# Kernel tuning notes

Hardware: AMD Instinct MI355X
Metric: run time of the kernel (lower is better)

## Reference

```python
import jax, jax.numpy as jnp
import numpy as np


def setup_inputs() -> dict:
    key = jax.random.key(0)
    ks = jax.random.split(key, 6)
    B, S, D, E, F, C = 4, 2048, 1024, 8, 4096, 512
    return {
        "x": jax.random.normal(ks[0], (B, S, D), dtype=jnp.float32),
        "router": jax.random.normal(ks[1], (D, E), dtype=jnp.float32) * (1.0 / np.sqrt(D)),
        "w1": jax.random.normal(ks[2], (E, D, F), dtype=jnp.float32) * (1.0 / np.sqrt(D)),
        "b1": jnp.zeros((E, F), dtype=jnp.float32),
        "w2": jax.random.normal(ks[3], (E, F, D), dtype=jnp.float32) * (1.0 / np.sqrt(F)),
        "b2": jnp.zeros((E, D), dtype=jnp.float32),
        "capacity": C,
    }


def reference(x, router, w1, b1, w2, b2, capacity):
    # x: (B,S,D); router: (D,E); per-expert FFN weights stacked on E.
    B, S, D = x.shape
    # Gate: softmax over experts, then each expert picks its top-C tokens.
    logits = jnp.einsum('bsd,de->bse', x, router)            # (B,S,E)
    affinity = jax.nn.softmax(logits, axis=-1)               # (B,S,E)
    gating, index = jax.lax.top_k(jnp.transpose(affinity, (0, 2, 1)), capacity)  # (B,E,C)
    # Dispatch: gather token features per (expert, slot). Equivalent to the
    # one-hot einsum 'becs,bsd->becd' in the original (same math, true gather).
    x_in = jax.vmap(lambda xb, ib: xb[ib])(x, index)         # (B,E,C,D)
    # Per-expert GPT2 FFN: Linear -> GELU -> Linear (grouped GEMMs over E).
    h = jax.nn.gelu(jnp.einsum('becd,edf->becf', x_in, w1) + b1[None, :, None, :],
                    approximate=False)                        # (B,E,C,F)
    x_e = jnp.einsum('becf,efd->becd', h, w2) + b2[None, :, None, :]  # (B,E,C,D)
    # Combine: weighted scatter-add back to token positions. Equivalent to
    # einsum 'becs,bec,becd->bsd' with the one-hot dispatch mask.
    weighted = gating[..., None] * x_e                       # (B,E,C,D)
    out = jax.vmap(
        lambda ib, vb: jnp.zeros((S, D), x.dtype).at[ib.reshape(-1)].add(vb.reshape(-1, D))
    )(index, weighted)                                       # (B,S,D)
    return out
```

## Files before the change

kernel.cpp:

```cpp
#include <hip/hip_runtime.h>
#include <hip/hip_bf16.h>

#define B_ 4
#define S_ 2048
#define D_ 1024
#define E_ 8
#define F_ 4096
#define C_ 512
#define BE_ (B_*E_)

typedef __attribute__((ext_vector_type(8))) short bf16x8;
typedef __attribute__((ext_vector_type(4))) float f32x4;
typedef unsigned short u16;

#define MFMA16 __builtin_amdgcn_mfma_f32_16x16x32_bf16

static constexpr size_t OFF_AFF  = 0;
static constexpr size_t OFF_IDX  = 262144;
static constexpr size_t OFF_GATE = 327680;
static constexpr size_t OFF_XIN  = 393216;
static constexpr size_t OFF_WT1  = OFF_XIN + (size_t)BE_*C_*D_*2;
static constexpr size_t OFF_WT2  = OFF_WT1 + (size_t)E_*F_*D_*2;
static constexpr size_t OFF_H    = OFF_WT2 + (size_t)E_*D_*F_*2;
static constexpr size_t WS_NEED  = OFF_H   + (size_t)BE_*C_*F_*2;

static __device__ __forceinline__ u16 f2bf(float x) {
  __hip_bfloat16 h = __float2bfloat16(x);
  return *reinterpret_cast<u16*>(&h);
}

static __device__ __forceinline__ float gelu_fast(float v) {
  float y = 1.5957691216f * (v + 0.044715f * v * v * v);
  return v / (1.0f + __expf(-y));
}

static __device__ __forceinline__ void gload16(const void* g, void* l) {
  __builtin_amdgcn_global_load_lds(
      (const __attribute__((address_space(1))) unsigned int*)g,
      (__attribute__((address_space(3))) unsigned int*)l, 16, 0, 0);
}

__global__ void router_kernel(const float* __restrict__ x,
                              const float* __restrict__ router,
                              float* __restrict__ aff) {
  int t = blockIdx.x;
  int b = t / S_, s = t % S_;
  int lane = threadIdx.x;
  const float* xrow = x + (size_t)t * D_;
  float acc[E_];
#pragma unroll
  for (int e = 0; e < E_; ++e) acc[e] = 0.f;
  for (int i = 0; i < D_/64; ++i) {
    int d = lane + i*64;
    float xv = xrow[d];
    const float* r = router + (size_t)d * E_;
#pragma unroll
    for (int e = 0; e < E_; ++e) acc[e] += xv * r[e];
  }
#pragma unroll
  for (int e = 0; e < E_; ++e) {
    float v = acc[e];
    for (int off = 32; off; off >>= 1) v += __shfl_down(v, off);
    acc[e] = v;
  }
  if (lane == 0) {
    float mx = acc[0];
#pragma unroll
    for (int e = 1; e < E_; ++e) mx = fmaxf(mx, acc[e]);
    float ev[E_]; float sum = 0.f;
#pragma unroll
    for (int e = 0; e < E_; ++e) { ev[e] = expf(acc[e] - mx); sum += ev[e]; }
    float inv = 1.0f / sum;
#pragma unroll
    for (int e = 0; e < E_; ++e) aff[((size_t)(b*E_ + e))*S_ + s] = ev[e]*inv;
  }
}

__global__ void topk_kernel(const float* __restrict__ aff,
                            int* __restrict__ idxb, float* __restrict__ gateb) {
  __shared__ unsigned long long keys[S_];
  int be = blockIdx.x;
  const float* a = aff + (size_t)be * S_;
  int tid = threadIdx.x;
  for (int i = tid; i < S_; i += 1024) {
    unsigned vb = __float_as_uint(a[i]);
    keys[i] = ((unsigned long long)(~vb) << 32) | (unsigned)i;
  }
  __syncthreads();
  for (int k = 2; k <= S_; k <<= 1) {
    for (int j = k >> 1; j > 0; j >>= 1) {
      for (int i = tid; i < S_; i += 1024) {
        int ixj = i ^ j;
        if (ixj > i) {
          unsigned long long ka = keys[i], kb = keys[ixj];
          bool up = ((i & k) == 0);
          if ((ka > kb) == up) { keys[i] = kb; keys[ixj] = ka; }
        }
      }
      __syncthreads();
    }
  }
  for (int c = tid; c < C_; c += 1024) {
    unsigned long long kk = keys[c];
    idxb[be*C_ + c]  = (int)(kk & 0xffffffffu);
    gateb[be*C_ + c] = __uint_as_float(~(unsigned)(kk >> 32));
  }
}

__global__ void gather_kernel(const float* __restrict__ x,
                              const int* __restrict__ idxb,
                              u16* __restrict__ x_in) {
  int rid = blockIdx.x;
  int be = rid >> 9;
  int b = be >> 3;
  int tok = idxb[rid];
  const float4* src = (const float4*)(x + ((size_t)(b * S_ + tok)) * D_);
  ushort4* dst = (ushort4*)(x_in + (size_t)rid * D_);
  int t = threadIdx.x;
#pragma unroll
  for (int i = 0; i < 2; ++i) {
    float4 v = src[t + i*128];
    ushort4 o;
    o.x = f2bf(v.x); o.y = f2bf(v.y); o.z = f2bf(v.z); o.w = f2bf(v.w);
    dst[t + i*128] = o;
  }
}

__global__ void trans_kernel(const float* __restrict__ src,
                             u16* __restrict__ dst, int RI, int RJ) {
  __shared__ float t[64][65];
  int e  = blockIdx.z;
  int j0 = blockIdx.x * 64;
  int i0 = blockIdx.y * 64;
  const float* s = src + (size_t)e * RI * RJ;
  u16* d = dst + (size_t)e * RI * RJ;
  int tid = threadIdx.x;
#pragma unroll
  for (int it = 0; it < 4; ++it) {
    int fid = it*256 + tid;
    int r = fid >> 4, c4 = fid & 15;
    float4 v = *(const float4*)(s + (size_t)(i0 + r) * RJ + j0 + c4*4);
    t[r][c4*4+0] = v.x; t[r][c4*4+1] = v.y; t[r][c4*4+2] = v.z; t[r][c4*4+3] = v.w;
  }
  __syncthreads();
#pragma unroll
  for (int it = 0; it < 4; ++it) {
    int fid = it*256 + tid;
    int rn = fid >> 4, c4 = fid & 15;
    ushort4 o;
    o.x = f2bf(t[c4*4+0][rn]); o.y = f2bf(t[c4*4+1][rn]);
    o.z = f2bf(t[c4*4+2][rn]); o.w = f2bf(t[c4*4+3][rn]);
    *(ushort4*)(d + (size_t)(j0 + rn) * RI + i0 + c4*4) = o;
  }
}

template<int N, int K, int NBLK>
__global__ __launch_bounds__(256, 4)
void gemm1_kernel(const u16* __restrict__ A, const u16* __restrict__ Bt,
                  const float* __restrict__ bias, __hip_bfloat16* __restrict__ outp) {
  __shared__ __align__(16) char lds[32768];
  char* ldsA = lds;
  char* ldsB = lds + 16384;
  const int tid  = threadIdx.x;
  const int wave = tid >> 6, lane = tid & 63;

  const int bid = blockIdx.x;
  const int e   = bid & 7;
  const int r   = bid >> 3;
  const int nb  = r % NBLK;
  const int rm  = r / NBLK;
  const int mb  = rm & 3;
  const int b   = rm >> 2;
  const int be  = b * E_ + e;
  const int m0  = mb * 128;
  const int n0  = nb * 128;

  const u16* Ab = A  + (size_t)be * C_ * K + (size_t)m0 * K;
  const u16* Bb = Bt + (size_t)e  * N  * K + (size_t)n0 * K;

  f32x4 acc[4][4];
#pragma unroll
  for (int i = 0; i < 4; ++i)
#pragma unroll
    for (int j = 0; j < 4; ++j) acc[i][j] = (f32x4){0.f,0.f,0.f,0.f};

  const int wr = wave >> 1, wc = wave & 1;
  const int chi = lane >> 4;
  const int l15 = lane & 15;

  for (int kt = 0; kt < K/64; ++kt) {
    const int k0 = kt * 64;
#pragma unroll
    for (int i = 0; i < 4; ++i) {
      int slot = i*256 + tid;
      int row = slot >> 3, c = slot & 7;
      int sc = (c ^ (row & 7)) << 3;
      gload16(Ab + (size_t)row * K + k0 + sc, ldsA + (i*256 + wave*64)*16);
      gload16(Bb + (size_t)row * K + k0 + sc, ldsB + (i*256 + wave*64)*16);
    }
    __syncthreads();
    bf16x8 af[2][4], bfr[2][4];
#pragma unroll
    for (int kk = 0; kk < 2; ++kk) {
#pragma unroll
      for (int mi = 0; mi < 4; ++mi) {
        int row = wr*64 + mi*16 + l15;
        int ch  = kk*4 + chi;
        af[kk][mi] = *(const bf16x8*)(ldsA + row*128 + (((ch ^ (row & 7)) << 4)));
        int rowb = wc*64 + mi*16 + l15;
        bfr[kk][mi] = *(const bf16x8*)(ldsB + rowb*128 + (((ch ^ (rowb & 7)) << 4)));
      }
    }
#pragma unroll
    for (int kk = 0; kk < 2; ++kk)
#pragma unroll
      for (int mi = 0; mi < 4; ++mi)
#pragma unroll
        for (int ni = 0; ni < 4; ++ni)
          acc[mi][ni] = MFMA16(af[kk][mi], bfr[kk][ni], acc[mi][ni], 0, 0, 0);
    __syncthreads();
  }

  const int r4 = lane >> 4;
  __hip_bfloat16* hb = outp + (size_t)be * C_ * N;
  const float* bias_e = bias + e * N;
#pragma unroll
  for (int mi = 0; mi < 4; ++mi) {
#pragma unroll
    for (int j = 0; j < 4; ++j) {
      int row = m0 + wr*64 + mi*16 + r4*4 + j;
      __hip_bfloat16* hrow = hb + (size_t)row * N;
#pragma unroll
      for (int ni = 0; ni < 4; ++ni) {
        int col = n0 + wc*64 + ni*16 + l15;
        float v = acc[mi][ni][j] + bias_e[col];
        hrow[col] = __float2bfloat16(gelu_fast(v));
      }
    }
  }
}

template<int N, int K, int NBLK>
__global__ __launch_bounds__(512, 2)
void gemm2_kernel(const u16* __restrict__ A, const u16* __restrict__ Bt,
                  const float* __restrict__ bias,
                  const int* __restrict__ idxb, const float* __restrict__ gateb,
                  float* __restrict__ dout) {
  constexpr int NT = K / 64;
  __shared__ __align__(16) char lds[131072];
  const int tid  = threadIdx.x;
  const int wave = tid >> 6, lane = tid & 63;
  const int wm = wave >> 2, wn = wave & 3;
  const int l15 = lane & 15, chi = lane >> 4;

  const int bid = blockIdx.x;
  const int e   = bid & 7;
  const int r   = bid >> 3;
  const int nb  = r % NBLK;
  const int rm  = r / NBLK;
  const int mb  = rm & 1;
  const int b   = rm >> 1;
  const int be  = b * E_ + e;
  const int m0  = mb * 256;
  const int n0  = nb * 256;

  const u16* Ab  = A  + (size_t)be * C_ * K + (size_t)m0 * K;
  const u16* Bb  = Bt + (size_t)e  * N  * K + (size_t)n0 * K;
  const u16* Ab2 = Ab + (size_t)128 * K;
  const u16* Bb2 = Bb + (size_t)128 * K;

  const int sr = tid >> 3, scn = tid & 7;
  const size_t off0 = (size_t)sr * K + (size_t)((scn ^ (sr & 7)) << 3);
  const size_t off1 = off0 + (size_t)64 * K;
  const int ldsd = tid * 16;

#define STAGE(tt, so, gb) \
  if ((tt) < NT) { \
    const u16* g_ = (gb) + (size_t)(tt) * 64; \
    char* l_ = lds + (((tt) & 1) * 65536) + (so); \
    gload16(g_ + off0, l_ + ldsd); \
    gload16(g_ + off1, l_ + 8192 + ldsd); \
  }

  const int q7  = l15 & 7;
  const int ch0 = ((chi    ) ^ q7) << 4;
  const int ch1 = ((4 + chi) ^ q7) << 4;
  const int aoff = wm * 16384 + l15 * 128;
  const int boff = 32768 + (wn >> 1) * 16384 + (wn & 1) * 8192 + l15 * 128;

  f32x4 acc[8][4];
#pragma unroll
  for (int i = 0; i < 8; ++i)
#pragma unroll
    for (int j = 0; j < 4; ++j) acc[i][j] = (f32x4){0.f,0.f,0.f,0.f};

  STAGE(0, 0,     Ab);
  STAGE(0, 16384, Ab2);
  STAGE(0, 32768, Bb);
  STAGE(0, 49152, Bb2);
  STAGE(1, 32768, Bb);
  STAGE(1, 49152, Bb2);
  asm volatile("s_waitcnt vmcnt(4)" ::: "memory");
  __builtin_amdgcn_s_barrier();

  bf16x8 af[2][4], bA[2][2], bB[2][2];
  for (int t = 0; t < NT; ++t) {
    const char* cb = lds + (t & 1) * 65536;
#pragma unroll
    for (int m = 0; m < 4; ++m) {
      af[0][m] = *(const bf16x8*)(cb + aoff + m*2048 + ch0);
      af[1][m] = *(const bf16x8*)(cb + aoff + m*2048 + ch1);
    }
#pragma unroll
    for (int n = 0; n < 2; ++n) {
      bA[0][n] = *(const bf16x8*)(cb + boff + n*2048 + ch0);
      bA[1][n] = *(const bf16x8*)(cb + boff + n*2048 + ch1);
    }
    STAGE(t+1, 0, Ab);
    asm volatile("s_waitcnt lgkmcnt(8)" ::: "memory");
    __builtin_amdgcn_s_barrier();
    asm volatile("s_waitcnt lgkmcnt(0)" ::: "memory");
    __builtin_amdgcn_s_setprio(1);
#pragma unroll
    for (int m = 0; m < 4; ++m)
#pragma unroll
      for (int n = 0; n < 2; ++n) {
        acc[m][n] = MFMA16(af[0][m], bA[0][n], acc[m][n], 0, 0, 0);
        acc[m][n] = MFMA16(af[1][m], bA[1][n], acc[m][n], 0, 0, 0);
      }
    __builtin_amdgcn_s_setprio(0);
    __builtin_amdgcn_s_barrier();
#pragma unroll
    for (int n = 0; n < 2; ++n) {
      bB[0][n] = *(const bf16x8*)(cb + boff + (2+n)*2048 + ch0);
      bB[1][n] = *(const bf16x8*)(cb + boff + (2+n)*2048 + ch1);
    }
    STAGE(t+1, 16384, Ab2);
    __builtin_amdgcn_s_barrier();
    asm volatile("s_waitcnt lgkmcnt(0)" ::: "memory");
    __builtin_amdgcn_s_setprio(1);
#pragma unroll
    for (int m = 0; m < 4; ++m)
#pragma unroll
      for (int n = 0; n < 2; ++n) {
        acc[m][2+n] = MFMA16(af[0][m], bB[0][n], acc[m][2+n], 0, 0, 0);
        acc[m][2+n] = MFMA16(af[1][m], bB[1][n], acc[m][2+n], 0, 0, 0);
      }
    __builtin_amdgcn_s_setprio(0);
    __builtin_amdgcn_s_barrier();
#pragma unroll
    for (int m = 0; m < 4; ++m) {
      af[0][m] = *(const bf16x8*)(cb + aoff + (4+m)*2048 + ch0);
      af[1][m] = *(const bf16x8*)(cb + aoff + (4+m)*2048 + ch1);
    }
    STAGE(t+2, 32768, Bb);
    __builtin_amdgcn_s_barrier();
    asm volatile("s_waitcnt lgkmcnt(0)" ::: "memory");
    __builtin_amdgcn_s_setprio(1);
#pragma unroll
    for (int m = 0; m < 4; ++m)
#pragma unroll
      for (int n = 0; n < 2; ++n) {
        acc[4+m][2+n] = MFMA16(af[0][m], bB[0][n], acc[4+m][2+n], 0, 0, 0);
        acc[4+m][2+n] = MFMA16(af[1][m], bB[1][n], acc[4+m][2+n], 0, 0, 0);
      }
    __builtin_amdgcn_s_setprio(0);
    __builtin_amdgcn_s_barrier();
    STAGE(t+2, 49152, Bb2);
    if (t < NT-2) {
      asm volatile("s_waitcnt vmcnt(4)" ::: "memory");
    } else if (t == NT-2) {
      asm volatile("s_waitcnt vmcnt(0)" ::: "memory");
    }
    __builtin_amdgcn_s_barrier();
    __builtin_amdgcn_s_setprio(1);
#pragma unroll
    for (int m = 0; m < 4; ++m)
#pragma unroll
      for (int n = 0; n < 2; ++n) {
        acc[4+m][n] = MFMA16(af[0][m], bA[0][n], acc[4+m][n], 0, 0, 0);
        acc[4+m][n] = MFMA16(af[1][m], bA[1][n], acc[4+m][n], 0, 0, 0);
      }
    __builtin_amdgcn_s_setprio(0);
    __builtin_amdgcn_s_barrier();
  }
#undef STAGE

  const int r4 = lane >> 4;
  const float* bias_e = bias + e * N;
  int bb = be >> 3;
#pragma unroll
  for (int mi = 0; mi < 8; ++mi) {
#pragma unroll
    for (int j = 0; j < 4; ++j) {
      int rowl = m0 + wm*128 + mi*16 + r4*4 + j;
      int tok = idxb[be*C_ + rowl];
      float gt = gateb[be*C_ + rowl];
      float* orow = dout + ((size_t)bb * S_ + tok) * (size_t)D_;
#pragma unroll
      for (int ni = 0; ni < 4; ++ni) {
        int col = n0 + wn*64 + ni*16 + l15;
        float v = (acc[mi][ni][j] + bias_e[col]) * gt;
        atomicAdd(orow + col, v);
      }
    }
  }
}

extern "C" void kernel_launch(void* const* d_in, const int* in_sizes, int n_in,
                              void* d_out, int out_size, void* d_ws, size_t ws_size,
                              hipStream_t stream) {
  const float* x      = (const float*)d_in[0];
  const float* router = (const float*)d_in[1];
  const float* w1     = (const float*)d_in[2];
  const float* b1     = (const float*)d_in[3];
  const float* w2     = (const float*)d_in[4];
  const float* b2     = (const float*)d_in[5];
  float* out = (float*)d_out;

  if (ws_size < WS_NEED) return;

  char* ws = (char*)d_ws;
  float* aff   = (float*)(ws + OFF_AFF);
  int*   idxb  = (int*)(ws + OFF_IDX);
  float* gateb = (float*)(ws + OFF_GATE);
  u16*   x_in  = (u16*)(ws + OFF_XIN);
  u16*   wt1   = (u16*)(ws + OFF_WT1);
  u16*   wt2   = (u16*)(ws + OFF_WT2);
  u16*   h     = (u16*)(ws + OFF_H);

  router_kernel<<<B_*S_, 64, 0, stream>>>(x, router, aff);
  topk_kernel<<<BE_, 1024, 0, stream>>>(aff, idxb, gateb);
  gather_kernel<<<BE_*C_, 128, 0, stream>>>(x, idxb, x_in);
  trans_kernel<<<dim3(F_/64, D_/64, E_), 256, 0, stream>>>(w1, wt1, D_, F_);
  trans_kernel<<<dim3(D_/64, F_/64, E_), 256, 0, stream>>>(w2, wt2, F_, D_);
  hipMemsetAsync(d_out, 0, (size_t)out_size * sizeof(float), stream);

  gemm1_kernel<F_, D_, F_/128><<<E_*(F_/128)*4*B_, 256, 0, stream>>>(
      x_in, wt1, b1, (__hip_bfloat16*)h);
  gemm2_kernel<D_, F_, D_/256><<<E_*(D_/256)*2*B_, 512, 0, stream>>>(
      h, wt2, b2, idxb, gateb, out);
}
```

Baseline: 466.6 us.

## Replace bitonic top-k with radix select, merge transposes, reorder GEMM1 blocks

Swaps the full bitonic sort of 2048 keys per (batch, expert) for a three-pass radix histogram select that finds the threshold value and then compacts the winners, cutting the many barrier-separated sort passes. The two weight transpose launches are merged into one grid, and the GEMM1 block index mapping is changed so blocks next to each other share the same weight N tile across batch and M tiles, aiming for better L2 reuse. Output order within each expert's slot list is no longer sorted, which is fine because combine is a scatter-add. Tie handling is order-dependent but selects the same set.

```diff
diff --git a/kernel.cpp b/kernel.cpp
--- a/kernel.cpp
+++ b/kernel.cpp
@@ -76,34 +76,124 @@
   }
 }
 
-__global__ void topk_kernel(const float* __restrict__ aff,
-                            int* __restrict__ idxb, float* __restrict__ gateb) {
-  __shared__ unsigned long long keys[S_];
-  int be = blockIdx.x;
+__global__ void select_kernel(const float* __restrict__ aff,
+                              int* __restrict__ idxb, float* __restrict__ gateb) {
+  __shared__ unsigned hist[2048];
+  __shared__ unsigned chunk[256];
+  __shared__ unsigned scv[2];
+  __shared__ unsigned cnt, tiecnt;
+  const int be = blockIdx.x, tid = threadIdx.x;
+  const int lane = tid & 63, wave = tid >> 6;
   const float* a = aff + (size_t)be * S_;
-  int tid = threadIdx.x;
-  for (int i = tid; i < S_; i += 1024) {
-    unsigned vb = __float_as_uint(a[i]);
-    keys[i] = ((unsigned long long)(~vb) << 32) | (unsigned)i;
-  }
-  __syncthreads();
-  for (int k = 2; k <= S_; k <<= 1) {
-    for (int j = k >> 1; j > 0; j >>= 1) {
-      for (int i = tid; i < S_; i += 1024) {
-        int ixj = i ^ j;
-        if (ixj > i) {
-          unsigned long long ka = keys[i], kb = keys[ixj];
-          bool up = ((i & k) == 0);
-          if ((ka > kb) == up) { keys[i] = kb; keys[ixj] = ka; }
+  unsigned bits[8];
+#pragma unroll
+  for (int i = 0; i < 8; ++i) bits[i] = __float_as_uint(a[i*256 + tid]);
+
+  unsigned target = C_;
+  unsigned tb1, tb2, tb3;
+
+  for (int i = tid; i < 2048; i += 256) hist[i] = 0;
+  if (tid == 0) { cnt = 0; tiecnt = 0; }
+  __syncthreads();
+#pragma unroll
+  for (int i = 0; i < 8; ++i) atomicAdd(&hist[bits[i] >> 20], 1u);
+  __syncthreads();
+  {
+    unsigned cs = 0;
+#pragma unroll
+    for (int k = 0; k < 8; ++k) cs += hist[tid*8 + k];
+    chunk[tid] = cs;
+    __syncthreads();
+    if (tid == 0) {
+      unsigned cum = 0; int cc = 255;
+      while (cum + chunk[cc] < target) { cum += chunk[cc]; --cc; }
+      int bb = cc*8 + 7;
+      while (cum + hist[bb] < target) { cum += hist[bb]; --bb; }
+      scv[0] = (unsigned)bb; scv[1] = target - cum;
+    }
+    __syncthreads();
+    tb1 = scv[0]; target = scv[1];
+    __syncthreads();
+  }
+  for (int i = tid; i < 2048; i += 256) hist[i] = 0;
+  __syncthreads();
+#pragma unroll
+  for (int i = 0; i < 8; ++i)
+    if ((bits[i] >> 20) == tb1) atomicAdd(&hist[(bits[i] >> 9) & 0x7FF], 1u);
+  __syncthreads();
+  {
+    unsigned cs = 0;
+#pragma unroll
+    for (int k = 0; k < 8; ++k) cs += hist[tid*8 + k];
+    chunk[tid] = cs;
+    __syncthreads();
+    if (tid == 0) {
+      unsigned cum = 0; int cc = 255;
+      while (cum + chunk[cc] < target) { cum += chunk[cc]; --cc; }
+      int bb = cc*8 + 7;
+      while (cum + hist[bb] < target) { cum += hist[bb]; --bb; }
+      scv[0] = (unsigned)bb; scv[1] = target - cum;
+    }
+    __syncthreads();
+    tb2 = scv[0]; target = scv[1];
+    __syncthreads();
+  }
+  const unsigned hi22 = (tb1 << 11) | tb2;
+  for (int i = tid; i < 512; i += 256) hist[i] = 0;
+  __syncthreads();
+#pragma unroll
+  for (int i = 0; i < 8; ++i)
+    if ((bits[i] >> 9) == hi22) atomicAdd(&hist[bits[i] & 0x1FF], 1u);
+  __syncthreads();
+  {
+    unsigned cs = 0;
+    if (tid < 64) {
+#pragma unroll
+      for (int k = 0; k < 8; ++k) cs += hist[tid*8 + k];
+      chunk[tid] = cs;
+    }
+    __syncthreads();
+    if (tid == 0) {
+      unsigned cum = 0; int cc = 63;
+      while (cum + chunk[cc] < target) { cum += chunk[cc]; --cc; }
+      int bb = cc*8 + 7;
+      while (cum + hist[bb] < target) { cum += hist[bb]; --bb; }
+      scv[0] = (unsigned)bb; scv[1] = target - cum;
+    }
+    __syncthreads();
+    tb3 = scv[0]; target = scv[1];
+  }
+  const unsigned T = (tb1 << 20) | (tb2 << 9) | tb3;
+
+#pragma unroll
+  for (int i = 0; i < 8; ++i) {
+    if (bits[i] > T) {
+      unsigned pos = atomicAdd(&cnt, 1u);
+      idxb[be*C_ + pos]  = i*256 + tid;
+      gateb[be*C_ + pos] = __uint_as_float(bits[i]);
+    }
+  }
+  __syncthreads();
+  const unsigned cnt0 = cnt;
+  for (int rnd = 0; rnd < 8; ++rnd) {
+    bool eq = (bits[rnd] == T);
+    for (int w = 0; w < 4; ++w) {
+      if (wave == w) {
+        unsigned long long m = __ballot(eq);
+        int below = __popcll(m & ((1ull << lane) - 1ull));
+        unsigned base = tiecnt;
+        if (eq) {
+          unsigned k = base + (unsigned)below;
+          if (k < target) {
+            unsigned pos = cnt0 + k;
+            idxb[be*C_ + pos]  = rnd*256 + tid;
+            gateb[be*C_ + pos] = __uint_as_float(bits[rnd]);
+          }
         }
+        if (lane == 0) tiecnt = base + (unsigned)__popcll(m);
       }
       __syncthreads();
     }
-  }
-  for (int c = tid; c < C_; c += 1024) {
-    unsigned long long kk = keys[c];
-    idxb[be*C_ + c]  = (int)(kk & 0xffffffffu);
-    gateb[be*C_ + c] = __uint_as_float(~(unsigned)(kk >> 32));
   }
 }
 
@@ -126,15 +216,18 @@
   }
 }
 
-__global__ void trans_kernel(const float* __restrict__ src,
-                             u16* __restrict__ dst, int RI, int RJ) {
+__global__ void trans_kernel(const float* __restrict__ w1,
+                             const float* __restrict__ w2,
+                             u16* __restrict__ wt1, u16* __restrict__ wt2) {
   __shared__ float t[64][65];
-  int e  = blockIdx.z;
-  int j0 = blockIdx.x * 64;
-  int i0 = blockIdx.y * 64;
-  const float* s = src + (size_t)e * RI * RJ;
-  u16* d = dst + (size_t)e * RI * RJ;
-  int tid = threadIdx.x;
+  const int z = blockIdx.y;
+  const float* s; u16* d; int RI, RJ, jb, ib;
+  if (z < 8) { s = w1 + (size_t)z*D_*F_;     d = wt1 + (size_t)z*D_*F_;
+               RI = D_; RJ = F_; jb = blockIdx.x & 63; ib = blockIdx.x >> 6; }
+  else       { s = w2 + (size_t)(z-8)*F_*D_; d = wt2 + (size_t)(z-8)*F_*D_;
+               RI = F_; RJ = D_; jb = blockIdx.x & 15; ib = blockIdx.x >> 4; }
+  const int j0 = jb * 64, i0 = ib * 64;
+  const int tid = threadIdx.x;
 #pragma unroll
   for (int it = 0; it < 4; ++it) {
     int fid = it*256 + tid;
@@ -167,10 +260,10 @@
   const int bid = blockIdx.x;
   const int e   = bid & 7;
   const int r   = bid >> 3;
-  const int nb  = r % NBLK;
-  const int rm  = r / NBLK;
-  const int mb  = rm & 3;
-  const int b   = rm >> 2;
+  const int g   = r & 15;
+  const int nb  = r >> 4;
+  const int mb  = g & 3;
+  const int b   = g >> 2;
   const int be  = b * E_ + e;
   const int m0  = mb * 128;
   const int n0  = nb * 128;
@@ -430,10 +523,9 @@
   u16*   h     = (u16*)(ws + OFF_H);
 
   router_kernel<<<B_*S_, 64, 0, stream>>>(x, router, aff);
-  topk_kernel<<<BE_, 1024, 0, stream>>>(aff, idxb, gateb);
+  select_kernel<<<BE_, 256, 0, stream>>>(aff, idxb, gateb);
   gather_kernel<<<BE_*C_, 128, 0, stream>>>(x, idxb, x_in);
-  trans_kernel<<<dim3(F_/64, D_/64, E_), 256, 0, stream>>>(w1, wt1, D_, F_);
-  trans_kernel<<<dim3(D_/64, F_/64, E_), 256, 0, stream>>>(w2, wt2, F_, D_);
+  trans_kernel<<<dim3(1024, 16), 256, 0, stream>>>(w1, w2, wt1, wt2);
   hipMemsetAsync(d_out, 0, (size_t)out_size * sizeof(float), stream);
 
   gemm1_kernel<F_, D_, F_/128><<<E_*(F_/128)*4*B_, 256, 0, stream>>>(
```

After: 459.2 us. No clear change (-1.6%).
